# Kernel optimization log

Hardware: AMD Instinct MI355X
Metric: run time of the kernel (lower is better)

The kernel has to match this reference:

```python
import jax, jax.numpy as jnp
import numpy as np

B, S, DIM = 1, 2048, 2048
H, KVH = 32, 8
D = DIM // H  # 64


def setup_inputs() -> dict:
    key = jax.random.key(0)
    ks = jax.random.split(key, 10)
    x = jax.random.normal(ks[0], (B, S, DIM), dtype=jnp.float32)
    # RoPE frequencies: theta=10000, per LLaMA
    inv_freq = 1.0 / (10000.0 ** (np.arange(0, D, 2, dtype=np.float32) / D))  # (D/2,)
    angles = np.arange(S, dtype=np.float32)[:, None] * inv_freq[None, :]      # (S, D/2)
    freqs_cos = jnp.asarray(np.cos(angles))
    freqs_sin = jnp.asarray(np.sin(angles))
    # causal mask (1,1,S,S), 1 = keep, 0 = masked
    mask = jnp.tril(jnp.ones((S, S), dtype=jnp.int32))[None, None, :, :]
    w = 0.02
    Wq = jax.random.normal(ks[1], (DIM, H * D), dtype=jnp.float32) * w
    bq = jnp.zeros((H * D,), dtype=jnp.float32)
    Wk = jax.random.normal(ks[2], (DIM, KVH * D), dtype=jnp.float32) * w
    bk = jnp.zeros((KVH * D,), dtype=jnp.float32)
    Wv = jax.random.normal(ks[3], (DIM, KVH * D), dtype=jnp.float32) * w
    bv = jnp.zeros((KVH * D,), dtype=jnp.float32)
    Wo = jax.random.normal(ks[4], (H * D, DIM), dtype=jnp.float32) * w
    bo = jnp.zeros((DIM,), dtype=jnp.float32)
    return {"x": x, "freqs_cos": freqs_cos, "freqs_sin": freqs_sin, "mask": mask,
            "Wq": Wq, "bq": bq, "Wk": Wk, "bk": bk, "Wv": Wv, "bv": bv, "Wo": Wo, "bo": bo}


def _rope(t, cos, sin):
    # t: (B, S, h, D) with D even; rotate consecutive pairs (real form of complex mult)
    tr = t.reshape(*t.shape[:-1], -1, 2)          # (B,S,h,D/2,2)
    c = cos[None, :, None, :]                     # (1,S,1,D/2)
    s = sin[None, :, None, :]
    o0 = tr[..., 0] * c - tr[..., 1] * s
    o1 = tr[..., 0] * s + tr[..., 1] * c
    return jnp.stack([o0, o1], axis=-1).reshape(t.shape)


def reference(x, freqs_cos, freqs_sin, mask, Wq, bq, Wk, bk, Wv, bv, Wo, bo):
    b, s, dim = x.shape
    scale = 1.0 / jnp.sqrt(jnp.asarray(D, dtype=x.dtype))
    q = (x @ Wq + bq).reshape(b, s, H, D)
    k = (x @ Wk + bk).reshape(b, s, KVH, D)
    v = (x @ Wv + bv).reshape(b, s, KVH, D)
    q = _rope(q, freqs_cos, freqs_sin)
    k = _rope(k, freqs_cos, freqs_sin)
    # GQA: repeat kv heads to match query heads
    rep = H // KVH
    k = jnp.repeat(k, rep, axis=2)
    v = jnp.repeat(v, rep, axis=2)
    # to (B, H, S, D)
    q = q.transpose(0, 2, 1, 3)
    k = k.transpose(0, 2, 1, 3)
    v = v.transpose(0, 2, 1, 3)
    scores = jnp.einsum('bhqd,bhkd->bhqk', q, k) * scale   # (B,H,S,S)
    neg = jnp.asarray(jnp.finfo(scores.dtype).min, dtype=scores.dtype)
    scores = jnp.where(mask == 0, neg, scores)
    attn = jax.nn.softmax(scores, axis=-1)
    out = jnp.einsum('bhqk,bhkd->bhqd', attn, v)            # (B,H,S,D)
    out = out.transpose(0, 2, 1, 3).reshape(b, s, H * D)
    return out @ Wo + bo
```

## Files before the change

### kernel.cpp

```cpp
#include <hip/hip_runtime.h>
#include <stdint.h>

#define S_LEN 2048
#define DIM   2048
#define NHEAD 32
#define KVHEAD 8
#define HDIM  64
#define NQKV  3072

typedef __attribute__((ext_vector_type(8))) __bf16 bf16x8;
typedef __attribute__((ext_vector_type(4))) float f32x4;
typedef __attribute__((ext_vector_type(8))) unsigned short u16x8;

__device__ __forceinline__ unsigned short f2bf(float f) {
  unsigned u = __builtin_bit_cast(unsigned, f);
  unsigned r = (u + 0x7FFFu + ((u >> 16) & 1u)) >> 16;
  return (unsigned short)r;
}
__device__ __forceinline__ float bf2f(unsigned short h) {
  unsigned u = ((unsigned)h) << 16;
  return __builtin_bit_cast(float, u);
}

__device__ __forceinline__ void gl_lds16(const void* g, void* l) {
  __builtin_amdgcn_global_load_lds(
      (const __attribute__((address_space(1))) unsigned*)g,
      (__attribute__((address_space(3))) unsigned*)l, 16, 0, 0);
}


__global__ void convert_x_kernel(const float* __restrict__ x,
                                 unsigned short* __restrict__ xb, int n4) {
  int i = blockIdx.x * blockDim.x + threadIdx.x;
  if (i >= n4) return;
  float4 v = ((const float4*)x)[i];
  ushort4 o;
  o.x = f2bf(v.x); o.y = f2bf(v.y); o.z = f2bf(v.z); o.w = f2bf(v.w);
  ((ushort4*)xb)[i] = o;
}

__global__ void bias_concat_kernel(const float* __restrict__ bq,
                                   const float* __restrict__ bk,
                                   const float* __restrict__ bv,
                                   float* __restrict__ bqkv) {
  int i = blockIdx.x * blockDim.x + threadIdx.x;
  if (i >= NQKV) return;
  bqkv[i] = (i < 2048) ? bq[i] : (i < 2560 ? bk[i - 2048] : bv[i - 2560]);
}

__global__ void transpose_f2b_kernel(const float* __restrict__ src, int R, int C,
                                     unsigned short* __restrict__ dst) {
  __shared__ float t[32][33];
  int bx = blockIdx.x * 32;
  int by = blockIdx.y * 32;
  int tx = threadIdx.x, ty = threadIdx.y;
#pragma unroll
  for (int j = 0; j < 32; j += 8)
    t[ty + j][tx] = src[(size_t)(by + ty + j) * C + bx + tx];
  __syncthreads();
#pragma unroll
  for (int j = 0; j < 32; j += 8)
    dst[(size_t)(bx + ty + j) * R + by + tx] = f2bf(t[tx][ty + j]);
}

__global__ void transpose_b2b_kernel(const unsigned short* __restrict__ src, int lds_,
                                     int R, int C,
                                     unsigned short* __restrict__ dst, int ldd) {
  __shared__ unsigned short t[32][33];
  int bx = blockIdx.x * 32;
  int by = blockIdx.y * 32;
  int tx = threadIdx.x, ty = threadIdx.y;
#pragma unroll
  for (int j = 0; j < 32; j += 8)
    t[ty + j][tx] = src[(size_t)(by + ty + j) * lds_ + bx + tx];
  __syncthreads();
#pragma unroll
  for (int j = 0; j < 32; j += 8)
    dst[(size_t)(bx + ty + j) * ldd + by + tx] = t[tx][ty + j];
}

__global__ void rope_kernel(unsigned short* __restrict__ qkv,
                            const float* __restrict__ fc,
                            const float* __restrict__ fs) {
  int idx = blockIdx.x * blockDim.x + threadIdx.x;
  int row = idx / 1280;
  int p   = idx - row * 1280;
  if (row >= S_LEN) return;
  int col = (p < 1024) ? (p * 2) : (2048 + (p - 1024) * 2);
  int fi = p & 31;
  float c  = fc[row * 32 + fi];
  float sn = fs[row * 32 + fi];
  unsigned* base = (unsigned*)(qkv + (size_t)row * NQKV + col);
  unsigned v = *base;
  float x0 = bf2f((unsigned short)(v & 0xFFFF));
  float x1 = bf2f((unsigned short)(v >> 16));
  unsigned short o0 = f2bf(x0 * c - x1 * sn);
  unsigned short o1 = f2bf(x0 * sn + x1 * c);
  *base = (unsigned)o0 | ((unsigned)o1 << 16);
}

template <int OUT_BF16>
__global__ __launch_bounds__(256) void gemm_bt_kernel(
    const unsigned short* __restrict__ A,
    const unsigned short* __restrict__ BT,
    const float* __restrict__ bias,
    void* __restrict__ Cc, int M, int N, int K) {
  __shared__ unsigned short As[2][128 * 32];
  __shared__ unsigned short Bs[2][128 * 32];
  const int tid = threadIdx.x;
  const int lane = tid & 63;
  const int wid = tid >> 6;
  const int wm = wid >> 1, wn = wid & 1;
  const int rowA0 = blockIdx.x * 128;
  const int rowB0 = blockIdx.y * 128;
  const int l15 = lane & 15, l4 = lane >> 4;

  f32x4 acc[4][4];
#pragma unroll
  for (int i = 0; i < 4; i++)
#pragma unroll
    for (int j = 0; j < 4; j++) acc[i][j] = (f32x4){0.f, 0.f, 0.f, 0.f};

  const int nK = K >> 5;

  auto stage = [&](int buf, int kt) {
#pragma unroll
    for (int j = 0; j < 2; ++j) {
      int chunk = wid * 2 + j;
      int o = chunk * 1024 + (lane << 4);
      int r = o >> 6;
      int cb = (o & 63) ^ ((r & 3) << 4);
      gl_lds16((const char*)A + ((size_t)(rowA0 + r) * K + kt * 32) * 2 + cb,
               (char*)&As[buf][0] + chunk * 1024);
      gl_lds16((const char*)BT + ((size_t)(rowB0 + r) * K + kt * 32) * 2 + cb,
               (char*)&Bs[buf][0] + chunk * 1024);
    }
  };

  stage(0, 0);
  __syncthreads();
  int buf = 0;

  for (int kt = 0; kt < nK; ++kt) {
    if (kt + 1 < nK) stage(buf ^ 1, kt + 1);

    bf16x8 af[4], bfr[4];
#pragma unroll
    for (int i = 0; i < 4; i++) {
      int ra = wm * 64 + i * 16 + l15;
      int rb = wn * 64 + i * 16 + l15;
      af[i]  = *(const bf16x8*)((const char*)&As[buf][0] + ra * 64 + ((l4 * 16) ^ ((ra & 3) << 4)));
      bfr[i] = *(const bf16x8*)((const char*)&Bs[buf][0] + rb * 64 + ((l4 * 16) ^ ((rb & 3) << 4)));
    }
#pragma unroll
    for (int i = 0; i < 4; i++)
#pragma unroll
      for (int j = 0; j < 4; j++)
        acc[i][j] = __builtin_amdgcn_mfma_f32_16x16x32_bf16(af[i], bfr[j], acc[i][j], 0, 0, 0);
    __syncthreads();
    buf ^= 1;
  }

#pragma unroll
  for (int i = 0; i < 4; i++) {
    int row0 = rowA0 + wm * 64 + i * 16 + l4 * 4;
#pragma unroll
    for (int j = 0; j < 4; j++) {
      int col = rowB0 + wn * 64 + j * 16 + l15;
      float bv_ = bias[col];
#pragma unroll
      for (int r = 0; r < 4; r++) {
        float v = acc[i][j][r] + bv_;
        size_t idx = (size_t)(row0 + r) * N + col;
        if (OUT_BF16) ((unsigned short*)Cc)[idx] = f2bf(v);
        else          ((float*)Cc)[idx] = v;
      }
    }
  }
}

__global__ __launch_bounds__(512) void attn_kernel(
    const unsigned short* __restrict__ qkv,
    const unsigned short* __restrict__ VT,
    unsigned short* __restrict__ O) {
  __shared__ unsigned short Ks[2][64 * 64];
  __shared__ unsigned short VTs[2][64 * 64];
  __shared__ unsigned short Ps[8][16 * 64];

  const int tid = threadIdx.x;
  const int lane = tid & 63;
  const int w = tid >> 6;
  const int l15 = lane & 15, l4 = lane >> 4;
  const int kvh = blockIdx.x >> 5;
  const int pr  = blockIdx.x & 31;
  const int h = kvh * 4 + (w >> 1);
  const int qsub = (w & 1) * 16;
  const int wbase = w << 10;

  u16x8 ones_u;
#pragma unroll
  for (int i = 0; i < 8; i++) ones_u[i] = 0x3F80;
  const bf16x8 onesf = __builtin_bit_cast(bf16x8, ones_u);

#pragma unroll 1
  for (int ph = 0; ph < 2; ++ph) {
    const int qt = ph ? pr : 63 - pr;
    const int nt = (qt >> 1) + 1;
    const int qbase = qt * 32;

    bf16x8 qf[2];
    {
      const unsigned short* qrow = qkv + (size_t)(qbase + qsub + l15) * NQKV + h * 64;
#pragma unroll
      for (int kf = 0; kf < 2; ++kf) {
        u16x8 raw = *(const u16x8*)(qrow + kf * 32 + l4 * 8);
        u16x8 sc;
#pragma unroll
        for (int i = 0; i < 8; i++) sc[i] = f2bf(bf2f(raw[i]) * 0.125f);
        qf[kf] = __builtin_bit_cast(bf16x8, sc);
      }
    }

    f32x4 oacc[4], lacc;
#pragma unroll
    for (int d = 0; d < 4; d++) oacc[d] = (f32x4){0.f, 0.f, 0.f, 0.f};
    lacc = (f32x4){0.f, 0.f, 0.f, 0.f};

    {
      int o = tid << 4;
      int r = o >> 7;
      int cb = (o & 127) ^ ((r & 7) << 4);
      gl_lds16((const char*)qkv + ((size_t)r * NQKV + 2048 + kvh * 64) * 2 + cb,
               (char*)&Ks[0][0] + wbase);
      gl_lds16((const char*)VT + ((size_t)(kvh * 64 + r) * S_LEN) * 2 + cb,
               (char*)&VTs[0][0] + wbase);
    }
    __syncthreads();

    int buf = 0;
    for (int t = 0; t < nt; ++t) {
      if (t + 1 < nt) {
        int kvb = (t + 1) * 64;
        int o = tid << 4;
        int r = o >> 7;
        int cb = (o & 127) ^ ((r & 7) << 4);
        gl_lds16((const char*)qkv + ((size_t)(kvb + r) * NQKV + 2048 + kvh * 64) * 2 + cb,
                 (char*)&Ks[buf ^ 1][0] + wbase);
        gl_lds16((const char*)VT + ((size_t)(kvh * 64 + r) * S_LEN + kvb) * 2 + cb,
                 (char*)&VTs[buf ^ 1][0] + wbase);
      }

      f32x4 sacc[4];
#pragma unroll
      for (int nf = 0; nf < 4; nf++) sacc[nf] = (f32x4){0.f, 0.f, 0.f, 0.f};
#pragma unroll
      for (int nf = 0; nf < 4; nf++) {
#pragma unroll
        for (int kf = 0; kf < 2; kf++) {
          int row = nf * 16 + l15;
          bf16x8 kb = *(const bf16x8*)((const char*)&Ks[buf][0] + row * 128 +
                                       ((kf * 64 + l4 * 16) ^ ((row & 7) << 4)));
          sacc[nf] = __builtin_amdgcn_mfma_f32_16x16x32_bf16(qf[kf], kb, sacc[nf], 0, 0, 0);
        }
      }

      if (t == nt - 1) {
        int kvb = t * 64;
#pragma unroll
        for (int nf = 0; nf < 4; nf++) {
          int kvpos = kvb + nf * 16 + l15;
#pragma unroll
          for (int r = 0; r < 4; r++) {
            int qpos = qbase + qsub + l4 * 4 + r;
            if (kvpos > qpos) sacc[nf][r] = -3.0e38f;
          }
        }
      }

#pragma unroll
      for (int nf = 0; nf < 4; nf++) {
#pragma unroll
        for (int r = 0; r < 4; r++) {
          float p = __expf(sacc[nf][r]);
          int rr = l4 * 4 + r;
          int b = ((nf * 16 + l15) * 2) ^ ((rr & 7) << 4);
          *(unsigned short*)((char*)&Ps[w][0] + rr * 128 + b) = f2bf(p);
        }
      }

#pragma unroll
      for (int kf = 0; kf < 2; kf++) {
        bf16x8 pf = *(const bf16x8*)((const char*)&Ps[w][0] + l15 * 128 +
                                     ((kf * 64 + l4 * 16) ^ ((l15 & 7) << 4)));
        lacc = __builtin_amdgcn_mfma_f32_16x16x32_bf16(pf, onesf, lacc, 0, 0, 0);
#pragma unroll
        for (int df = 0; df < 4; df++) {
          int row = df * 16 + l15;
          bf16x8 vb = *(const bf16x8*)((const char*)&VTs[buf][0] + row * 128 +
                                       ((kf * 64 + l4 * 16) ^ ((row & 7) << 4)));
          oacc[df] = __builtin_amdgcn_mfma_f32_16x16x32_bf16(pf, vb, oacc[df], 0, 0, 0);
        }
      }
      __syncthreads();
      buf ^= 1;
    }

#pragma unroll
    for (int r = 0; r < 4; r++) {
      float inv = 1.0f / lacc[r];
      int qpos = qbase + qsub + l4 * 4 + r;
#pragma unroll
      for (int df = 0; df < 4; df++)
        O[(size_t)qpos * DIM + h * 64 + df * 16 + l15] = f2bf(oacc[df][r] * inv);
    }
  }
}

extern "C" void kernel_launch(void* const* d_in, const int* in_sizes, int n_in,
                              void* d_out, int out_size, void* d_ws, size_t ws_size,
                              hipStream_t stream) {
  const float* x  = (const float*)d_in[0];
  const float* fc = (const float*)d_in[1];
  const float* fs = (const float*)d_in[2];
  const float* Wq = (const float*)d_in[4];
  const float* bq = (const float*)d_in[5];
  const float* Wk = (const float*)d_in[6];
  const float* bk = (const float*)d_in[7];
  const float* Wv = (const float*)d_in[8];
  const float* bv = (const float*)d_in[9];
  const float* Wo = (const float*)d_in[10];
  const float* bo = (const float*)d_in[11];
  float* out = (float*)d_out;

  char* ws = (char*)d_ws;
  unsigned short* xb    = (unsigned short*)(ws + 0);
  unsigned short* WqkvT = (unsigned short*)(ws + 8388608);
  unsigned short* WoT   = (unsigned short*)(ws + 20971520);
  float*          bqkv  = (float*)(ws + 29360128);
  unsigned short* qkv   = (unsigned short*)(ws + 29372416);
  unsigned short* VT    = WqkvT;
  unsigned short* attn  = xb;

  convert_x_kernel<<<4096, 256, 0, stream>>>(x, xb, 2048 * 2048 / 4);
  bias_concat_kernel<<<12, 256, 0, stream>>>(bq, bk, bv, bqkv);
  dim3 tb(32, 8);
  transpose_f2b_kernel<<<dim3(64, 64), tb, 0, stream>>>(Wq, 2048, 2048, WqkvT);
  transpose_f2b_kernel<<<dim3(16, 64), tb, 0, stream>>>(Wk, 2048, 512, WqkvT + (size_t)2048 * 2048);
  transpose_f2b_kernel<<<dim3(16, 64), tb, 0, stream>>>(Wv, 2048, 512, WqkvT + (size_t)2560 * 2048);
  transpose_f2b_kernel<<<dim3(64, 64), tb, 0, stream>>>(Wo, 2048, 2048, WoT);

  gemm_bt_kernel<1><<<dim3(16, 24), 256, 0, stream>>>(xb, WqkvT, bqkv, qkv, 2048, 3072, 2048);
  rope_kernel<<<(2048 * 1280) / 256, 256, 0, stream>>>(qkv, fc, fs);
  transpose_b2b_kernel<<<dim3(16, 64), tb, 0, stream>>>(qkv + 2560, NQKV, 2048, 512, VT, 2048);
  attn_kernel<<<256, 512, 0, stream>>>(qkv, VT, attn);
  gemm_bt_kernel<0><<<dim3(16, 16), 256, 0, stream>>>(attn, WoT, bo, out, 2048, 2048, 2048);
}
```

Before: 266.5 us.

## Merge weight transposes, split-K GEMM warps, triple-buffer attention with exp2

The four weight-transpose launches become a single kernel. The GEMM now uses 512 threads with a 64-wide K step, where two groups of warps each handle half of K and reduce through LDS in the epilogue. The attention kernel moves from double to triple buffering, using explicit vmcnt waits and a raw barrier in place of the trailing syncthreads. It also folds log2(e) into the Q scale so exp2 can be used, and replaces the MFMA row-sum with per-lane sums followed by a shuffle reduction. These changes aim to cut launch overhead, barrier stalls and load latency, at the cost of more LDS per block and subtler synchronization.

```diff
diff --git a/kernel.cpp b/kernel.cpp
--- a/kernel.cpp
+++ b/kernel.cpp
@@ -11,6 +11,12 @@
 typedef __attribute__((ext_vector_type(8))) __bf16 bf16x8;
 typedef __attribute__((ext_vector_type(4))) float f32x4;
 typedef __attribute__((ext_vector_type(8))) unsigned short u16x8;
+
+#if __has_builtin(__builtin_amdgcn_exp2f)
+#define EXP2F(x) __builtin_amdgcn_exp2f(x)
+#else
+#define EXP2F(x) exp2f(x)
+#endif
 
 __device__ __forceinline__ unsigned short f2bf(float f) {
   unsigned u = __builtin_bit_cast(unsigned, f);
@@ -48,19 +54,27 @@
   bqkv[i] = (i < 2048) ? bq[i] : (i < 2560 ? bk[i - 2048] : bv[i - 2560]);
 }
 
-__global__ void transpose_f2b_kernel(const float* __restrict__ src, int R, int C,
-                                     unsigned short* __restrict__ dst) {
+__global__ void transpose_weights_kernel(const float* __restrict__ Wq,
+                                         const float* __restrict__ Wk,
+                                         const float* __restrict__ Wv,
+                                         const float* __restrict__ Wo,
+                                         unsigned short* __restrict__ WqkvT,
+                                         unsigned short* __restrict__ WoT) {
   __shared__ float t[32][33];
-  int bx = blockIdx.x * 32;
-  int by = blockIdx.y * 32;
+  int bx = blockIdx.x, by = blockIdx.y;
+  const float* src; int C, sc, dbase; unsigned short* dst;
+  if (bx < 64)      { src = Wq; C = 2048; sc = bx * 32;        dst = WqkvT; dbase = sc; }
+  else if (bx < 80) { src = Wk; C = 512;  sc = (bx - 64) * 32; dst = WqkvT; dbase = 2048 + sc; }
+  else if (bx < 96) { src = Wv; C = 512;  sc = (bx - 80) * 32; dst = WqkvT; dbase = 2560 + sc; }
+  else              { src = Wo; C = 2048; sc = (bx - 96) * 32; dst = WoT;   dbase = sc; }
   int tx = threadIdx.x, ty = threadIdx.y;
 #pragma unroll
   for (int j = 0; j < 32; j += 8)
-    t[ty + j][tx] = src[(size_t)(by + ty + j) * C + bx + tx];
+    t[ty + j][tx] = src[(size_t)(by * 32 + ty + j) * C + sc + tx];
   __syncthreads();
 #pragma unroll
   for (int j = 0; j < 32; j += 8)
-    dst[(size_t)(bx + ty + j) * R + by + tx] = f2bf(t[tx][ty + j]);
+    dst[(size_t)(dbase + ty + j) * 2048 + by * 32 + tx] = f2bf(t[tx][ty + j]);
 }
 
 __global__ void transpose_b2b_kernel(const unsigned short* __restrict__ src, int lds_,
@@ -100,20 +114,22 @@
 }
 
 template <int OUT_BF16>
-__global__ __launch_bounds__(256) void gemm_bt_kernel(
+__global__ __launch_bounds__(512) void gemm_bt_kernel(
     const unsigned short* __restrict__ A,
     const unsigned short* __restrict__ BT,
     const float* __restrict__ bias,
     void* __restrict__ Cc, int M, int N, int K) {
-  __shared__ unsigned short As[2][128 * 32];
-  __shared__ unsigned short Bs[2][128 * 32];
+  __shared__ char smem[65536];
   const int tid = threadIdx.x;
   const int lane = tid & 63;
   const int wid = tid >> 6;
-  const int wm = wid >> 1, wn = wid & 1;
+  const int kh = wid >> 2;
+  const int wsub = wid & 3;
+  const int wm = wsub >> 1, wn = wsub & 1;
   const int rowA0 = blockIdx.x * 128;
   const int rowB0 = blockIdx.y * 128;
   const int l15 = lane & 15, l4 = lane >> 4;
+  const int kcol = kh * 64 + l4 * 16;
 
   f32x4 acc[4][4];
 #pragma unroll
@@ -121,19 +137,18 @@
 #pragma unroll
     for (int j = 0; j < 4; j++) acc[i][j] = (f32x4){0.f, 0.f, 0.f, 0.f};
 
-  const int nK = K >> 5;
+  const int nK = K >> 6;
 
   auto stage = [&](int buf, int kt) {
-#pragma unroll
-    for (int j = 0; j < 2; ++j) {
-      int chunk = wid * 2 + j;
-      int o = chunk * 1024 + (lane << 4);
-      int r = o >> 6;
-      int cb = (o & 63) ^ ((r & 3) << 4);
-      gl_lds16((const char*)A + ((size_t)(rowA0 + r) * K + kt * 32) * 2 + cb,
-               (char*)&As[buf][0] + chunk * 1024);
-      gl_lds16((const char*)BT + ((size_t)(rowB0 + r) * K + kt * 32) * 2 + cb,
-               (char*)&Bs[buf][0] + chunk * 1024);
+    const char* Ab = (const char*)A + ((size_t)rowA0 * K + (size_t)kt * 64) * 2;
+    const char* Bb = (const char*)BT + ((size_t)rowB0 * K + (size_t)kt * 64) * 2;
+#pragma unroll
+    for (int h = 0; h < 2; ++h) {
+      int o = h * 8192 + tid * 16;
+      int r = o >> 7;
+      int cb = (o & 127) ^ ((r & 7) << 4);
+      gl_lds16(Ab + (size_t)r * (K * 2) + cb, smem + buf * 16384 + o);
+      gl_lds16(Bb + (size_t)r * (K * 2) + cb, smem + 32768 + buf * 16384 + o);
     }
   };
 
@@ -149,8 +164,8 @@
     for (int i = 0; i < 4; i++) {
       int ra = wm * 64 + i * 16 + l15;
       int rb = wn * 64 + i * 16 + l15;
-      af[i]  = *(const bf16x8*)((const char*)&As[buf][0] + ra * 64 + ((l4 * 16) ^ ((ra & 3) << 4)));
-      bfr[i] = *(const bf16x8*)((const char*)&Bs[buf][0] + rb * 64 + ((l4 * 16) ^ ((rb & 3) << 4)));
+      af[i]  = *(const bf16x8*)(smem + buf * 16384 + ra * 128 + (kcol ^ ((ra & 7) << 4)));
+      bfr[i] = *(const bf16x8*)(smem + 32768 + buf * 16384 + rb * 128 + (kcol ^ ((rb & 7) << 4)));
     }
 #pragma unroll
     for (int i = 0; i < 4; i++)
@@ -161,19 +176,31 @@
     buf ^= 1;
   }
 
-#pragma unroll
-  for (int i = 0; i < 4; i++) {
-    int row0 = rowA0 + wm * 64 + i * 16 + l4 * 4;
-#pragma unroll
-    for (int j = 0; j < 4; j++) {
-      int col = rowB0 + wn * 64 + j * 16 + l15;
-      float bv_ = bias[col];
-#pragma unroll
-      for (int r = 0; r < 4; r++) {
-        float v = acc[i][j][r] + bv_;
-        size_t idx = (size_t)(row0 + r) * N + col;
-        if (OUT_BF16) ((unsigned short*)Cc)[idx] = f2bf(v);
-        else          ((float*)Cc)[idx] = v;
+  f32x4* eps = (f32x4*)smem;
+  if (kh == 1) {
+#pragma unroll
+    for (int i = 0; i < 4; i++)
+#pragma unroll
+      for (int j = 0; j < 4; j++)
+        eps[wsub * 1024 + (i * 4 + j) * 64 + lane] = acc[i][j];
+  }
+  __syncthreads();
+  if (kh == 0) {
+#pragma unroll
+    for (int i = 0; i < 4; i++) {
+      int row0 = rowA0 + wm * 64 + i * 16 + l4 * 4;
+#pragma unroll
+      for (int j = 0; j < 4; j++) {
+        f32x4 oth = eps[wsub * 1024 + (i * 4 + j) * 64 + lane];
+        int col = rowB0 + wn * 64 + j * 16 + l15;
+        float bv_ = bias[col];
+#pragma unroll
+        for (int r = 0; r < 4; r++) {
+          float v = acc[i][j][r] + oth[r] + bv_;
+          size_t idx = (size_t)(row0 + r) * N + col;
+          if (OUT_BF16) ((unsigned short*)Cc)[idx] = f2bf(v);
+          else          ((float*)Cc)[idx] = v;
+        }
       }
     }
   }
@@ -183,8 +210,8 @@
     const unsigned short* __restrict__ qkv,
     const unsigned short* __restrict__ VT,
     unsigned short* __restrict__ O) {
-  __shared__ unsigned short Ks[2][64 * 64];
-  __shared__ unsigned short VTs[2][64 * 64];
+  __shared__ unsigned short Ks[3][64 * 64];
+  __shared__ unsigned short VTs[3][64 * 64];
   __shared__ unsigned short Ps[8][16 * 64];
 
   const int tid = threadIdx.x;
@@ -195,12 +222,17 @@
   const int pr  = blockIdx.x & 31;
   const int h = kvh * 4 + (w >> 1);
   const int qsub = (w & 1) * 16;
-  const int wbase = w << 10;
-
-  u16x8 ones_u;
-#pragma unroll
-  for (int i = 0; i < 8; i++) ones_u[i] = 0x3F80;
-  const bf16x8 onesf = __builtin_bit_cast(bf16x8, ones_u);
+
+  auto issue = [&](int buf, int t) {
+    int kvb = t * 64;
+    int o = tid << 4;
+    int r = o >> 7;
+    int cb = (o & 127) ^ ((r & 7) << 4);
+    gl_lds16((const char*)qkv + ((size_t)(kvb + r) * NQKV + 2048 + kvh * 64) * 2 + cb,
+             (char*)&Ks[buf][0] + o);
+    gl_lds16((const char*)VT + ((size_t)(kvh * 64 + r) * S_LEN + kvb) * 2 + cb,
+             (char*)&VTs[buf][0] + o);
+  };
 
 #pragma unroll 1
   for (int ph = 0; ph < 2; ++ph) {
@@ -216,39 +248,29 @@
         u16x8 raw = *(const u16x8*)(qrow + kf * 32 + l4 * 8);
         u16x8 sc;
 #pragma unroll
-        for (int i = 0; i < 8; i++) sc[i] = f2bf(bf2f(raw[i]) * 0.125f);
+        for (int i = 0; i < 8; i++) sc[i] = f2bf(bf2f(raw[i]) * 0.1803368801111f);
         qf[kf] = __builtin_bit_cast(bf16x8, sc);
       }
     }
 
-    f32x4 oacc[4], lacc;
+    f32x4 oacc[4];
+    float lsum[4];
 #pragma unroll
     for (int d = 0; d < 4; d++) oacc[d] = (f32x4){0.f, 0.f, 0.f, 0.f};
-    lacc = (f32x4){0.f, 0.f, 0.f, 0.f};
-
-    {
-      int o = tid << 4;
-      int r = o >> 7;
-      int cb = (o & 127) ^ ((r & 7) << 4);
-      gl_lds16((const char*)qkv + ((size_t)r * NQKV + 2048 + kvh * 64) * 2 + cb,
-               (char*)&Ks[0][0] + wbase);
-      gl_lds16((const char*)VT + ((size_t)(kvh * 64 + r) * S_LEN) * 2 + cb,
-               (char*)&VTs[0][0] + wbase);
-    }
+#pragma unroll
+    for (int r = 0; r < 4; r++) lsum[r] = 0.f;
+
     __syncthreads();
-
-    int buf = 0;
+    issue(0, 0);
+    if (nt > 1) issue(1, 1);
+
     for (int t = 0; t < nt; ++t) {
-      if (t + 1 < nt) {
-        int kvb = (t + 1) * 64;
-        int o = tid << 4;
-        int r = o >> 7;
-        int cb = (o & 127) ^ ((r & 7) << 4);
-        gl_lds16((const char*)qkv + ((size_t)(kvb + r) * NQKV + 2048 + kvh * 64) * 2 + cb,
-                 (char*)&Ks[buf ^ 1][0] + wbase);
-        gl_lds16((const char*)VT + ((size_t)(kvh * 64 + r) * S_LEN + kvb) * 2 + cb,
-                 (char*)&VTs[buf ^ 1][0] + wbase);
-      }
+      if (t + 1 < nt) { asm volatile("s_waitcnt vmcnt(2)" ::: "memory"); }
+      else            { asm volatile("s_waitcnt vmcnt(0)" ::: "memory"); }
+      __builtin_amdgcn_s_barrier();
+      asm volatile("" ::: "memory");
+      if (t + 2 < nt) issue((t + 2) % 3, t + 2);
+      const int buf = t % 3;
 
       f32x4 sacc[4];
 #pragma unroll
@@ -281,7 +303,8 @@
       for (int nf = 0; nf < 4; nf++) {
 #pragma unroll
         for (int r = 0; r < 4; r++) {
-          float p = __expf(sacc[nf][r]);
+          float p = EXP2F(sacc[nf][r]);
+          lsum[r] += p;
           int rr = l4 * 4 + r;
           int b = ((nf * 16 + l15) * 2) ^ ((rr & 7) << 4);
           *(unsigned short*)((char*)&Ps[w][0] + rr * 128 + b) = f2bf(p);
@@ -292,7 +315,6 @@
       for (int kf = 0; kf < 2; kf++) {
         bf16x8 pf = *(const bf16x8*)((const char*)&Ps[w][0] + l15 * 128 +
                                      ((kf * 64 + l4 * 16) ^ ((l15 & 7) << 4)));
-        lacc = __builtin_amdgcn_mfma_f32_16x16x32_bf16(pf, onesf, lacc, 0, 0, 0);
 #pragma unroll
         for (int df = 0; df < 4; df++) {
           int row = df * 16 + l15;
@@ -301,13 +323,17 @@
           oacc[df] = __builtin_amdgcn_mfma_f32_16x16x32_bf16(pf, vb, oacc[df], 0, 0, 0);
         }
       }
-      __syncthreads();
-      buf ^= 1;
     }
 
 #pragma unroll
     for (int r = 0; r < 4; r++) {
-      float inv = 1.0f / lacc[r];
+#pragma unroll
+      for (int off = 1; off < 16; off <<= 1) lsum[r] += __shfl_xor(lsum[r], off, 64);
+    }
+
+#pragma unroll
+    for (int r = 0; r < 4; r++) {
+      float inv = 1.0f / lsum[r];
       int qpos = qbase + qsub + l4 * 4 + r;
 #pragma unroll
       for (int df = 0; df < 4; df++)
@@ -344,14 +370,11 @@
   convert_x_kernel<<<4096, 256, 0, stream>>>(x, xb, 2048 * 2048 / 4);
   bias_concat_kernel<<<12, 256, 0, stream>>>(bq, bk, bv, bqkv);
   dim3 tb(32, 8);
-  transpose_f2b_kernel<<<dim3(64, 64), tb, 0, stream>>>(Wq, 2048, 2048, WqkvT);
-  transpose_f2b_kernel<<<dim3(16, 64), tb, 0, stream>>>(Wk, 2048, 512, WqkvT + (size_t)2048 * 2048);
-  transpose_f2b_kernel<<<dim3(16, 64), tb, 0, stream>>>(Wv, 2048, 512, WqkvT + (size_t)2560 * 2048);
-  transpose_f2b_kernel<<<dim3(64, 64), tb, 0, stream>>>(Wo, 2048, 2048, WoT);
-
-  gemm_bt_kernel<1><<<dim3(16, 24), 256, 0, stream>>>(xb, WqkvT, bqkv, qkv, 2048, 3072, 2048);
+  transpose_weights_kernel<<<dim3(160, 64), tb, 0, stream>>>(Wq, Wk, Wv, Wo, WqkvT, WoT);
+
+  gemm_bt_kernel<1><<<dim3(16, 24), 512, 0, stream>>>(xb, WqkvT, bqkv, qkv, 2048, 3072, 2048);
   rope_kernel<<<(2048 * 1280) / 256, 256, 0, stream>>>(qkv, fc, fs);
   transpose_b2b_kernel<<<dim3(16, 64), tb, 0, stream>>>(qkv + 2560, NQKV, 2048, 512, VT, 2048);
   attn_kernel<<<256, 512, 0, stream>>>(qkv, VT, attn);
-  gemm_bt_kernel<0><<<dim3(16, 16), 256, 0, stream>>>(attn, WoT, bo, out, 2048, 2048, 2048);
-}
+  gemm_bt_kernel<0><<<dim3(16, 16), 512, 0, stream>>>(attn, WoT, bo, out, 2048, 2048, 2048);
+}
```

Measured after the change: 238.5 us. 1.12x faster.
